# Kernel tuning notes

Hardware: AMD Instinct MI355X
Metric: run time of the kernel (lower is better)

The kernel has to match this reference:

```python
import jax, jax.numpy as jnp
import numpy as np

HEAD_DIM = 64
MASK_PENALTY = 1000000.0


def setup_inputs() -> dict:
    key = jax.random.key(0)
    kq, kk, kv, ki = jax.random.split(key, 4)
    B, H, S, D = 32, 16, 512, HEAD_DIM
    E, CAP = 8, 4  # n_experts = hidden(1024)//128, capacity per expert
    Q = jax.random.normal(kq, (B, H, S, D), dtype=jnp.float32)
    K = jax.random.normal(kk, (B, H, S, D), dtype=jnp.float32)
    V = jax.random.normal(kv, (B, H, S, D), dtype=jnp.float32)
    idx_list = jax.random.randint(ki, (E, CAP), 0, B)  # per-expert routed batch indices
    mask = jnp.ones((B, S), dtype=jnp.float32)
    return {"Q": Q, "K": K, "V": V, "idx_list": idx_list, "mask": mask}


def reference(Q, K, V, idx_list, mask):
    # Per-expert grouped attention: gather routed batch rows, QK^T, masked
    # softmax, AV. Dropout is identity in eval mode.
    scale = 1.0 / jnp.sqrt(jnp.asarray(HEAD_DIM, dtype=Q.dtype))

    def expert_attn(idx_e):
        q = Q[idx_e]            # [cap, H, S, D]
        k = K[idx_e]
        v = V[idx_e]
        m = mask[idx_e]         # [cap, S]
        dot = jnp.einsum('bhsd,bhtd->bhst', q, k) * scale
        dot = dot - MASK_PENALTY * (1.0 - m[:, None, None, :])
        p = jax.nn.softmax(dot, axis=-1)
        return jnp.einsum('bhst,bhtd->bhsd', p, v)  # [cap, H, S, D]

    X = jax.vmap(expert_attn)(idx_list)  # [E, cap, H, S, D]
    return X
```

## Files before the change

kernel.cpp:

```cpp
#include <hip/hip_runtime.h>
#include <math.h>


typedef _Float16 f16x8 __attribute__((ext_vector_type(8)));
typedef _Float16 f16x4 __attribute__((ext_vector_type(4)));
typedef _Float16 f16x2 __attribute__((ext_vector_type(2)));
typedef float    f32x4 __attribute__((ext_vector_type(4)));

#define MFMA16(a, b, c) __builtin_amdgcn_mfma_f32_16x16x32_f16((a), (b), (c), 0, 0, 0)

constexpr int Hh = 16;
constexpr int Ss = 512;
constexpr int Dd = 64;
constexpr int QB = 128;
constexpr int KVB = 64;
constexpr float QS = 0.125f * 1.44269504088896f;
constexpr float BM = 1000000.0f * 1.44269504088896f;

union U8 { f16x8 v; f16x2 h[4]; };

__device__ __forceinline__ int SW(int row, int col) {
  return row * 64 + (col ^ ((row & 7) << 3));
}

__device__ __forceinline__ f16x2 pkrtz(float a, float b) {
  auto t = __builtin_amdgcn_cvt_pkrtz(a, b);
  return *(f16x2*)&t;
}

__global__ __launch_bounds__(256) void sparse_attn_kernel(
    const float* __restrict__ Q, const float* __restrict__ K,
    const float* __restrict__ V, const int* __restrict__ idx,
    const float* __restrict__ mask, float* __restrict__ out) {
  const int tid  = threadIdx.x;
  const int lane = tid & 63;
  const int wv   = tid >> 6;
  const int r    = lane & 15;
  const int g    = lane >> 4;

  const int phys = blockIdx.x;
  const int G    = (phys & 7) | ((phys >> 5) << 3);
  const int qb   = (phys >> 3) & 3;
  const int h    = G & 15;
  const int ec   = G >> 4;
  const int b    = idx[ec];

  __shared__ _Float16 Ks[64 * 64];
  __shared__ _Float16 VTs[64 * 64];
  __shared__ float    maskS[Ss];

  const size_t bh = ((size_t)b * Hh + h) * (size_t)Ss * Dd;
  const float* Qb = Q + bh;
  const float* Kb = K + bh;
  const float* Vb = V + bh;
  const float* mrow = mask + (size_t)b * Ss;

  *(float2*)&maskS[2 * tid] = *(const float2*)(mrow + 2 * tid);

  const int q0 = qb * QB + wv * 32;

  f16x8 qf[2][2];
#pragma unroll
  for (int mi = 0; mi < 2; ++mi)
#pragma unroll
    for (int kk = 0; kk < 2; ++kk) {
      const float* qp = Qb + (size_t)(q0 + mi * 16 + r) * Dd + kk * 32 + g * 8;
      float4 x0 = *(const float4*)qp;
      float4 x1 = *(const float4*)(qp + 4);
      U8 u;
      u.h[0] = pkrtz(x0.x * QS, x0.y * QS);
      u.h[1] = pkrtz(x0.z * QS, x0.w * QS);
      u.h[2] = pkrtz(x1.x * QS, x1.y * QS);
      u.h[3] = pkrtz(x1.z * QS, x1.w * QS);
      qf[mi][kk] = u.v;
    }

  f16x8 ones;
#pragma unroll
  for (int e = 0; e < 8; ++e) ones[e] = (_Float16)1.0f;

  f32x4 oacc[2][4];
#pragma unroll
  for (int mi = 0; mi < 2; ++mi)
#pragma unroll
    for (int nj = 0; nj < 4; ++nj) oacc[mi][nj] = (f32x4){0.f, 0.f, 0.f, 0.f};
  f32x4 lacc[2] = {(f32x4){0.f, 0.f, 0.f, 0.f}, (f32x4){0.f, 0.f, 0.f, 0.f}};

  float4 kx0[2], kx1[2];
  float  vv[2][8];

#define KV_ISSUE(KV0)                                                        \
  {                                                                          \
    _Pragma("unroll")                                                        \
    for (int it = 0; it < 2; ++it) {                                         \
      int j = it * 256 + tid;                                                \
      const float* kp_ = Kb + (size_t)((KV0) + (j >> 3)) * Dd + (j & 7) * 8; \
      kx0[it] = *(const float4*)kp_;                                         \
      kx1[it] = *(const float4*)(kp_ + 4);                                   \
    }                                                                        \
    _Pragma("unroll")                                                        \
    for (int it = 0; it < 2; ++it) {                                         \
      int oct = (tid >> 6) + 4 * it;                                         \
      int kb1 = (oct >> 2) * 16 + (oct & 3) * 4;                             \
      const float* vp = Vb + (size_t)((KV0) + kb1) * Dd + (tid & 63);        \
      _Pragma("unroll")                                                      \
      for (int jj = 0; jj < 4; ++jj) {                                       \
        vv[it][jj]     = vp[(size_t)jj * Dd];                                \
        vv[it][jj + 4] = vp[(size_t)(jj + 32) * Dd];                         \
      }                                                                      \
    }                                                                        \
  }

  KV_ISSUE(0)

  for (int t = 0; t < Ss / KVB; ++t) {
    const int kv0 = t * KVB;
    if (t) __syncthreads();

#pragma unroll
    for (int it = 0; it < 2; ++it) {
      int j = it * 256 + tid;
      U8 u;
      u.h[0] = pkrtz(kx0[it].x, kx0[it].y);
      u.h[1] = pkrtz(kx0[it].z, kx0[it].w);
      u.h[2] = pkrtz(kx1[it].x, kx1[it].y);
      u.h[3] = pkrtz(kx1[it].z, kx1[it].w);
      *(f16x8*)&Ks[SW(j >> 3, (j & 7) * 8)] = u.v;
    }
#pragma unroll
    for (int it = 0; it < 2; ++it) {
      int oct = (tid >> 6) + 4 * it;
      int dim = tid & 63;
      U8 u;
      u.h[0] = pkrtz(vv[it][0], vv[it][1]);
      u.h[1] = pkrtz(vv[it][2], vv[it][3]);
      u.h[2] = pkrtz(vv[it][4], vv[it][5]);
      u.h[3] = pkrtz(vv[it][6], vv[it][7]);
      *(f16x8*)&VTs[SW(dim, oct * 8)] = u.v;
    }
    __syncthreads();

    if (t < Ss / KVB - 1) KV_ISSUE(kv0 + KVB)

    f32x4 bv[4];
#pragma unroll
    for (int nj = 0; nj < 4; ++nj) {
      f32x4 mv = *(const f32x4*)&maskS[kv0 + nj * 16 + g * 4];
      bv[nj][0] = mv[0] * BM - BM;
      bv[nj][1] = mv[1] * BM - BM;
      bv[nj][2] = mv[2] * BM - BM;
      bv[nj][3] = mv[3] * BM - BM;
    }

    f32x4 sf[2][4];
#pragma unroll
    for (int nj = 0; nj < 4; ++nj) { sf[0][nj] = bv[nj]; sf[1][nj] = bv[nj]; }
    __builtin_amdgcn_s_setprio(1);
#pragma unroll
    for (int nj = 0; nj < 4; ++nj)
#pragma unroll
      for (int kk = 0; kk < 2; ++kk) {
        f16x8 kf = *(const f16x8*)&Ks[SW(nj * 16 + r, kk * 32 + g * 8)];
        sf[0][nj] = MFMA16(kf, qf[0][kk], sf[0][nj]);
        sf[1][nj] = MFMA16(kf, qf[1][kk], sf[1][nj]);
      }
    __builtin_amdgcn_s_setprio(0);

    f16x8 pf[2][2];
#pragma unroll
    for (int mi = 0; mi < 2; ++mi) {
      float p[4][4];
#pragma unroll
      for (int nj = 0; nj < 4; ++nj)
#pragma unroll
        for (int rg = 0; rg < 4; ++rg)
          p[nj][rg] = __builtin_amdgcn_exp2f(sf[mi][nj][rg]);
#pragma unroll
      for (int kk = 0; kk < 2; ++kk) {
        U8 u;
        u.h[0] = pkrtz(p[kk][0], p[kk][1]);
        u.h[1] = pkrtz(p[kk][2], p[kk][3]);
        u.h[2] = pkrtz(p[kk + 2][0], p[kk + 2][1]);
        u.h[3] = pkrtz(p[kk + 2][2], p[kk + 2][3]);
        pf[mi][kk] = u.v;
      }
    }

    __builtin_amdgcn_s_setprio(1);
#pragma unroll
    for (int kk = 0; kk < 2; ++kk) {
      lacc[0] = MFMA16(pf[0][kk], ones, lacc[0]);
      lacc[1] = MFMA16(pf[1][kk], ones, lacc[1]);
#pragma unroll
      for (int nj = 0; nj < 4; ++nj) {
        f16x8 vf = *(const f16x8*)&VTs[SW(nj * 16 + r, kk * 32 + g * 8)];
        oacc[0][nj] = MFMA16(pf[0][kk], vf, oacc[0][nj]);
        oacc[1][nj] = MFMA16(pf[1][kk], vf, oacc[1][nj]);
      }
    }
    __builtin_amdgcn_s_setprio(0);
  }

  float* ob = out + ((size_t)ec * Hh + h) * (size_t)Ss * Dd;
#pragma unroll
  for (int mi = 0; mi < 2; ++mi) {
    float i4[4];
#pragma unroll
    for (int rg = 0; rg < 4; ++rg) i4[rg] = 1.0f / lacc[mi][rg];
#pragma unroll
    for (int nj = 0; nj < 4; ++nj)
#pragma unroll
      for (int rg = 0; rg < 4; ++rg) {
        int row = q0 + mi * 16 + g * 4 + rg;
        int dim = nj * 16 + r;
        ob[(size_t)row * Dd + dim] = oacc[mi][nj][rg] * i4[rg];
      }
  }
}

extern "C" void kernel_launch(void* const* d_in, const int* in_sizes, int n_in,
                              void* d_out, int out_size, void* d_ws, size_t ws_size,
                              hipStream_t stream) {
  const float* Q    = (const float*)d_in[0];
  const float* K    = (const float*)d_in[1];
  const float* V    = (const float*)d_in[2];
  const int*   idx  = (const int*)d_in[3];
  const float* mask = (const float*)d_in[4];
  float* out = (float*)d_out;
  dim3 grid(2048), block(256);
  hipLaunchKernelGGL(sparse_attn_kernel, grid, block, 0, stream,
                     Q, K, V, idx, mask, out);
}
```

Before: 64.98 us.

## Double-buffer K/V shared-memory tiles to drop one barrier per iteration

Shared K and transposed V tiles become double-buffered. The next tile is converted and written into the alternate buffer after the current tile's compute, so each loop iteration needs one barrier instead of two. This is meant to cut synchronization stalls and let the LDS writes overlap with other waves' compute. LDS use per block doubles, to about 34KB, which could lower occupancy.

```diff
diff --git a/kernel.cpp b/kernel.cpp
--- a/kernel.cpp
+++ b/kernel.cpp
@@ -14,6 +14,7 @@
 constexpr int Dd = 64;
 constexpr int QB = 128;
 constexpr int KVB = 64;
+constexpr int NT = Ss / KVB;
 constexpr float QS = 0.125f * 1.44269504088896f;
 constexpr float BM = 1000000.0f * 1.44269504088896f;
 
@@ -45,8 +46,8 @@
   const int ec   = G >> 4;
   const int b    = idx[ec];
 
-  __shared__ _Float16 Ks[64 * 64];
-  __shared__ _Float16 VTs[64 * 64];
+  __shared__ _Float16 Ks[2][64 * 64];
+  __shared__ _Float16 VTs[2][64 * 64];
   __shared__ float    maskS[Ss];
 
   const size_t bh = ((size_t)b * Hh + h) * (size_t)Ss * Dd;
@@ -111,36 +112,40 @@
     }                                                                        \
   }
 
+#define STAGE_WRITE(B)                                                       \
+  {                                                                          \
+    _Pragma("unroll")                                                        \
+    for (int it = 0; it < 2; ++it) {                                         \
+      int j = it * 256 + tid;                                                \
+      U8 u;                                                                  \
+      u.h[0] = pkrtz(kx0[it].x, kx0[it].y);                                  \
+      u.h[1] = pkrtz(kx0[it].z, kx0[it].w);                                  \
+      u.h[2] = pkrtz(kx1[it].x, kx1[it].y);                                  \
+      u.h[3] = pkrtz(kx1[it].z, kx1[it].w);                                  \
+      *(f16x8*)&Ks[B][SW(j >> 3, (j & 7) * 8)] = u.v;                        \
+    }                                                                        \
+    _Pragma("unroll")                                                        \
+    for (int it = 0; it < 2; ++it) {                                         \
+      int oct = (tid >> 6) + 4 * it;                                         \
+      int dim = tid & 63;                                                    \
+      U8 u;                                                                  \
+      u.h[0] = pkrtz(vv[it][0], vv[it][1]);                                  \
+      u.h[1] = pkrtz(vv[it][2], vv[it][3]);                                  \
+      u.h[2] = pkrtz(vv[it][4], vv[it][5]);                                  \
+      u.h[3] = pkrtz(vv[it][6], vv[it][7]);                                  \
+      *(f16x8*)&VTs[B][SW(dim, oct * 8)] = u.v;                              \
+    }                                                                        \
+  }
+
   KV_ISSUE(0)
-
-  for (int t = 0; t < Ss / KVB; ++t) {
+  STAGE_WRITE(0)
+  __syncthreads();
+
+  int cur = 0;
+  for (int t = 0; t < NT; ++t) {
     const int kv0 = t * KVB;
-    if (t) __syncthreads();
-
-#pragma unroll
-    for (int it = 0; it < 2; ++it) {
-      int j = it * 256 + tid;
-      U8 u;
-      u.h[0] = pkrtz(kx0[it].x, kx0[it].y);
-      u.h[1] = pkrtz(kx0[it].z, kx0[it].w);
-      u.h[2] = pkrtz(kx1[it].x, kx1[it].y);
-      u.h[3] = pkrtz(kx1[it].z, kx1[it].w);
-      *(f16x8*)&Ks[SW(j >> 3, (j & 7) * 8)] = u.v;
-    }
-#pragma unroll
-    for (int it = 0; it < 2; ++it) {
-      int oct = (tid >> 6) + 4 * it;
-      int dim = tid & 63;
-      U8 u;
-      u.h[0] = pkrtz(vv[it][0], vv[it][1]);
-      u.h[1] = pkrtz(vv[it][2], vv[it][3]);
-      u.h[2] = pkrtz(vv[it][4], vv[it][5]);
-      u.h[3] = pkrtz(vv[it][6], vv[it][7]);
-      *(f16x8*)&VTs[SW(dim, oct * 8)] = u.v;
-    }
-    __syncthreads();
-
-    if (t < Ss / KVB - 1) KV_ISSUE(kv0 + KVB)
+
+    if (t < NT - 1) KV_ISSUE(kv0 + KVB)
 
     f32x4 bv[4];
 #pragma unroll
@@ -160,7 +165,7 @@
     for (int nj = 0; nj < 4; ++nj)
 #pragma unroll
       for (int kk = 0; kk < 2; ++kk) {
-        f16x8 kf = *(const f16x8*)&Ks[SW(nj * 16 + r, kk * 32 + g * 8)];
+        f16x8 kf = *(const f16x8*)&Ks[cur][SW(nj * 16 + r, kk * 32 + g * 8)];
         sf[0][nj] = MFMA16(kf, qf[0][kk], sf[0][nj]);
         sf[1][nj] = MFMA16(kf, qf[1][kk], sf[1][nj]);
       }
@@ -193,12 +198,18 @@
       lacc[1] = MFMA16(pf[1][kk], ones, lacc[1]);
 #pragma unroll
       for (int nj = 0; nj < 4; ++nj) {
-        f16x8 vf = *(const f16x8*)&VTs[SW(nj * 16 + r, kk * 32 + g * 8)];
+        f16x8 vf = *(const f16x8*)&VTs[cur][SW(nj * 16 + r, kk * 32 + g * 8)];
         oacc[0][nj] = MFMA16(pf[0][kk], vf, oacc[0][nj]);
         oacc[1][nj] = MFMA16(pf[1][kk], vf, oacc[1][nj]);
       }
     }
     __builtin_amdgcn_s_setprio(0);
+
+    if (t < NT - 1) {
+      STAGE_WRITE(cur ^ 1)
+      __syncthreads();
+    }
+    cur ^= 1;
   }
 
   float* ob = out + ((size_t)ec * Hh + h) * (size_t)Ss * Dd;
```

Result: slower. 67.93 us (+4.5%).

## Double query tile to 256 rows with 512-thread blocks sharing each K/V tile

Applied to the files above, without the earlier changes.

Each block now handles 256 query rows with 8 waves instead of 128 rows with 4 waves, which halves the grid. Every K/V tile staged in LDS is therefore reused by twice as many queries, cutting redundant global loads and fp16 conversion of K/V. Each thread now stages one K row chunk and one V column chunk per tile. The mask bias is precomputed once into shared memory, and the prefetch of the next tile is issued before the barrier. The cost is fewer blocks in flight, which could lower occupancy or leave the GPU less evenly loaded.

```diff
diff --git a/kernel.cpp b/kernel.cpp
--- a/kernel.cpp
+++ b/kernel.cpp
@@ -12,8 +12,9 @@
 constexpr int Hh = 16;
 constexpr int Ss = 512;
 constexpr int Dd = 64;
-constexpr int QB = 128;
+constexpr int QB = 256;
 constexpr int KVB = 64;
+constexpr int NT = Ss / KVB;
 constexpr float QS = 0.125f * 1.44269504088896f;
 constexpr float BM = 1000000.0f * 1.44269504088896f;
 
@@ -28,7 +29,7 @@
   return *(f16x2*)&t;
 }
 
-__global__ __launch_bounds__(256) void sparse_attn_kernel(
+__global__ __launch_bounds__(512) void sparse_attn_kernel(
     const float* __restrict__ Q, const float* __restrict__ K,
     const float* __restrict__ V, const int* __restrict__ idx,
     const float* __restrict__ mask, float* __restrict__ out) {
@@ -39,15 +40,15 @@
   const int g    = lane >> 4;
 
   const int phys = blockIdx.x;
-  const int G    = (phys & 7) | ((phys >> 5) << 3);
-  const int qb   = (phys >> 3) & 3;
+  const int G    = (phys & 7) | ((phys >> 4) << 3);
+  const int qb   = (phys >> 3) & 1;
   const int h    = G & 15;
   const int ec   = G >> 4;
   const int b    = idx[ec];
 
   __shared__ _Float16 Ks[64 * 64];
   __shared__ _Float16 VTs[64 * 64];
-  __shared__ float    maskS[Ss];
+  __shared__ float    biasS[Ss];
 
   const size_t bh = ((size_t)b * Hh + h) * (size_t)Ss * Dd;
   const float* Qb = Q + bh;
@@ -55,7 +56,7 @@
   const float* Vb = V + bh;
   const float* mrow = mask + (size_t)b * Ss;
 
-  *(float2*)&maskS[2 * tid] = *(const float2*)(mrow + 2 * tid);
+  biasS[tid] = mrow[tid] * BM - BM;
 
   const int q0 = qb * QB + wv * 32;
 
@@ -86,71 +87,54 @@
     for (int nj = 0; nj < 4; ++nj) oacc[mi][nj] = (f32x4){0.f, 0.f, 0.f, 0.f};
   f32x4 lacc[2] = {(f32x4){0.f, 0.f, 0.f, 0.f}, (f32x4){0.f, 0.f, 0.f, 0.f}};
 
-  float4 kx0[2], kx1[2];
-  float  vv[2][8];
+  float4 kx0, kx1;
+  float  vv[8];
 
 #define KV_ISSUE(KV0)                                                        \
   {                                                                          \
+    const float* kp_ = Kb + (size_t)((KV0) + (tid >> 3)) * Dd + (tid & 7) * 8;\
+    kx0 = *(const float4*)kp_;                                               \
+    kx1 = *(const float4*)(kp_ + 4);                                         \
+    int oct = tid >> 6;                                                      \
+    int kb1 = (oct >> 2) * 16 + (oct & 3) * 4;                               \
+    const float* vp = Vb + (size_t)((KV0) + kb1) * Dd + (tid & 63);          \
     _Pragma("unroll")                                                        \
-    for (int it = 0; it < 2; ++it) {                                         \
-      int j = it * 256 + tid;                                                \
-      const float* kp_ = Kb + (size_t)((KV0) + (j >> 3)) * Dd + (j & 7) * 8; \
-      kx0[it] = *(const float4*)kp_;                                         \
-      kx1[it] = *(const float4*)(kp_ + 4);                                   \
+    for (int jj = 0; jj < 4; ++jj) {                                         \
+      vv[jj]     = vp[(size_t)jj * Dd];                                      \
+      vv[jj + 4] = vp[(size_t)(jj + 32) * Dd];                               \
     }                                                                        \
-    _Pragma("unroll")                                                        \
-    for (int it = 0; it < 2; ++it) {                                         \
-      int oct = (tid >> 6) + 4 * it;                                         \
-      int kb1 = (oct >> 2) * 16 + (oct & 3) * 4;                             \
-      const float* vp = Vb + (size_t)((KV0) + kb1) * Dd + (tid & 63);        \
-      _Pragma("unroll")                                                      \
-      for (int jj = 0; jj < 4; ++jj) {                                       \
-        vv[it][jj]     = vp[(size_t)jj * Dd];                                \
-        vv[it][jj + 4] = vp[(size_t)(jj + 32) * Dd];                         \
-      }                                                                      \
-    }                                                                        \
+  }
+
+#define STAGE_WRITE()                                                        \
+  {                                                                          \
+    U8 u;                                                                    \
+    u.h[0] = pkrtz(kx0.x, kx0.y);                                            \
+    u.h[1] = pkrtz(kx0.z, kx0.w);                                            \
+    u.h[2] = pkrtz(kx1.x, kx1.y);                                            \
+    u.h[3] = pkrtz(kx1.z, kx1.w);                                            \
+    *(f16x8*)&Ks[SW(tid >> 3, (tid & 7) * 8)] = u.v;                         \
+    U8 u2;                                                                   \
+    u2.h[0] = pkrtz(vv[0], vv[1]);                                           \
+    u2.h[1] = pkrtz(vv[2], vv[3]);                                           \
+    u2.h[2] = pkrtz(vv[4], vv[5]);                                           \
+    u2.h[3] = pkrtz(vv[6], vv[7]);                                           \
+    *(f16x8*)&VTs[SW(tid & 63, (tid >> 6) * 8)] = u2.v;                      \
   }
 
   KV_ISSUE(0)
 
-  for (int t = 0; t < Ss / KVB; ++t) {
+  for (int t = 0; t < NT; ++t) {
     const int kv0 = t * KVB;
     if (t) __syncthreads();
 
-#pragma unroll
-    for (int it = 0; it < 2; ++it) {
-      int j = it * 256 + tid;
-      U8 u;
-      u.h[0] = pkrtz(kx0[it].x, kx0[it].y);
-      u.h[1] = pkrtz(kx0[it].z, kx0[it].w);
-      u.h[2] = pkrtz(kx1[it].x, kx1[it].y);
-      u.h[3] = pkrtz(kx1[it].z, kx1[it].w);
-      *(f16x8*)&Ks[SW(j >> 3, (j & 7) * 8)] = u.v;
-    }
-#pragma unroll
-    for (int it = 0; it < 2; ++it) {
-      int oct = (tid >> 6) + 4 * it;
-      int dim = tid & 63;
-      U8 u;
-      u.h[0] = pkrtz(vv[it][0], vv[it][1]);
-      u.h[1] = pkrtz(vv[it][2], vv[it][3]);
-      u.h[2] = pkrtz(vv[it][4], vv[it][5]);
-      u.h[3] = pkrtz(vv[it][6], vv[it][7]);
-      *(f16x8*)&VTs[SW(dim, oct * 8)] = u.v;
-    }
+    STAGE_WRITE()
+    if (t < NT - 1) KV_ISSUE(kv0 + KVB)
     __syncthreads();
 
-    if (t < Ss / KVB - 1) KV_ISSUE(kv0 + KVB)
-
     f32x4 bv[4];
 #pragma unroll
-    for (int nj = 0; nj < 4; ++nj) {
-      f32x4 mv = *(const f32x4*)&maskS[kv0 + nj * 16 + g * 4];
-      bv[nj][0] = mv[0] * BM - BM;
-      bv[nj][1] = mv[1] * BM - BM;
-      bv[nj][2] = mv[2] * BM - BM;
-      bv[nj][3] = mv[3] * BM - BM;
-    }
+    for (int nj = 0; nj < 4; ++nj)
+      bv[nj] = *(const f32x4*)&biasS[kv0 + nj * 16 + g * 4];
 
     f32x4 sf[2][4];
 #pragma unroll
@@ -227,7 +211,7 @@
   const int*   idx  = (const int*)d_in[3];
   const float* mask = (const float*)d_in[4];
   float* out = (float*)d_out;
-  dim3 grid(2048), block(256);
+  dim3 grid(1024), block(512);
   hipLaunchKernelGGL(sparse_attn_kernel, grid, block, 0, stream,
                      Q, K, V, idx, mask, out);
 }
```

Result: no change. 65.11 us (+0.2%).
